# Kernel tuning notes

Measured on AMD Instinct MI355X. Metric: run time of the kernel, lower is better.

Reference implementation:

```python
import jax, jax.numpy as jnp
import numpy as np

N_NODES = 100000


def _gcn_norm(edge_index, num_nodes):
    # PyG GCNConv default: add self-loops, symmetric normalization.
    src, dst = edge_index[0], edge_index[1]
    loop = jnp.arange(num_nodes, dtype=src.dtype)
    src = jnp.concatenate([src, loop])
    dst = jnp.concatenate([dst, loop])
    deg = jax.ops.segment_sum(jnp.ones_like(dst, dtype=jnp.float32), dst,
                              num_segments=num_nodes)
    dinv = jnp.where(deg > 0, jax.lax.rsqrt(jnp.maximum(deg, 1.0)), 0.0)
    norm = dinv[src] * dinv[dst]  # [E + N]
    return src, dst, norm


def _gcn_layer(x, src, dst, norm, W, b, num_nodes):
    h = x @ W                              # [N, out]
    msg = h[src] * norm[:, None]           # gather + scale, [E+N, out]
    agg = jax.ops.segment_sum(msg, dst, num_segments=num_nodes)  # scatter-add
    return agg + b


def setup_inputs() -> dict:
    key = jax.random.key(0)
    ks = jax.random.split(key, 12)
    in_c, hid = 64, 128
    dims = [in_c, hid, hid // 2, hid // 4, hid // 8, 1]
    x = jax.random.normal(ks[0], (N_NODES, in_c), dtype=jnp.float32)
    edge_index = jax.random.randint(ks[1], (2, 1600000), 0, N_NODES,
                                    dtype=jnp.int64)
    inp = {"x": x, "edge_index": edge_index}
    for i in range(5):
        fan_in = dims[i]
        s = 1.0 / np.sqrt(fan_in)
        inp[f"W{i+1}"] = jax.random.uniform(ks[2 + 2 * i], (dims[i], dims[i + 1]),
                                            minval=-s, maxval=s,
                                            dtype=jnp.float32)
        inp[f"b{i+1}"] = jnp.zeros((dims[i + 1],), dtype=jnp.float32)
    return inp


def reference(x, edge_index, W1, b1, W2, b2, W3, b3, W4, b4, W5, b5):
    num_nodes = x.shape[0]
    src, dst, norm = _gcn_norm(edge_index, num_nodes)
    h = _gcn_layer(x, src, dst, norm, W1, b1, num_nodes)
    h = jax.nn.relu(h)
    h = _gcn_layer(h, src, dst, norm, W2, b2, num_nodes)
    h = jax.nn.relu(h)
    h = _gcn_layer(h, src, dst, norm, W3, b3, num_nodes)
    h = jax.nn.relu(h)
    h = _gcn_layer(h, src, dst, norm, W4, b4, num_nodes)
    h = jax.nn.relu(h)
    h = _gcn_layer(h, src, dst, norm, W5, b5, num_nodes)
    return h
```

## Files before the change

### kernel.cpp

```cpp
#include <hip/hip_runtime.h>
#include <math.h>


#define NBIN_MAX 256
#define BSHIFT 9
#define BINW 512
#define CHUNK 2048

__global__ __launch_bounds__(256) void k_hist(const int* __restrict__ dst, int E,
                                              int nbin, int* __restrict__ binCnt) {
    __shared__ int h[NBIN_MAX];
    int t = threadIdx.x;
    for (int i = t; i < nbin; i += 256) h[i] = 0;
    __syncthreads();
    int e4 = (blockIdx.x * 256 + t) * 4;
    int stride = gridDim.x * 256 * 4;
    for (; e4 + 3 < E; e4 += stride) {
        int4 d = *(const int4*)&dst[e4];
        atomicAdd(&h[d.x >> BSHIFT], 1);
        atomicAdd(&h[d.y >> BSHIFT], 1);
        atomicAdd(&h[d.z >> BSHIFT], 1);
        atomicAdd(&h[d.w >> BSHIFT], 1);
    }
    for (; e4 < E; ++e4) atomicAdd(&h[dst[e4] >> BSHIFT], 1);
    __syncthreads();
    for (int i = t; i < nbin; i += 256)
        if (h[i]) atomicAdd(&binCnt[i], h[i]);
}

__global__ __launch_bounds__(256) void k_binscan(const int* __restrict__ binCnt,
                                                 int nbin, int* __restrict__ binBase,
                                                 int* __restrict__ binCur) {
    __shared__ int sh[256];
    int t = threadIdx.x;
    int v = (t < nbin) ? binCnt[t] : 0;
    sh[t] = v;
    __syncthreads();
    for (int d = 1; d < 256; d <<= 1) {
        int u = (t >= d) ? sh[t - d] : 0;
        __syncthreads();
        sh[t] += u;
        __syncthreads();
    }
    int ex = sh[t] - v;
    if (t < nbin) { binBase[t] = ex; binCur[t] = ex; }
    if (t == nbin - 1) binBase[nbin] = sh[t];
}

__global__ __launch_bounds__(256) void k_binfill(const int* __restrict__ src,
                                                 const int* __restrict__ dst, int E,
                                                 int nbin, int* __restrict__ binCur,
                                                 unsigned* __restrict__ tmp) {
    __shared__ int h[NBIN_MAX];
    __shared__ int res[NBIN_MAX];
    int t = threadIdx.x;
    int e0 = blockIdx.x * CHUNK;
    int e1 = min(e0 + CHUNK, E);
    int vend = e0 + ((e1 - e0) & ~3);
    for (int i = t; i < nbin; i += 256) h[i] = 0;
    __syncthreads();
    for (int e = e0 + t * 4; e < vend; e += 1024) {
        int4 d = *(const int4*)&dst[e];
        atomicAdd(&h[d.x >> BSHIFT], 1);
        atomicAdd(&h[d.y >> BSHIFT], 1);
        atomicAdd(&h[d.z >> BSHIFT], 1);
        atomicAdd(&h[d.w >> BSHIFT], 1);
    }
    for (int e = vend + t; e < e1; e += 256)
        atomicAdd(&h[dst[e] >> BSHIFT], 1);
    __syncthreads();
    for (int i = t; i < nbin; i += 256)
        res[i] = h[i] ? atomicAdd(&binCur[i], h[i]) : 0;
    __syncthreads();
    for (int i = t; i < nbin; i += 256) h[i] = 0;
    __syncthreads();
    for (int e = e0 + t * 4; e < vend; e += 1024) {
        int4 d = *(const int4*)&dst[e];
        int4 s = *(const int4*)&src[e];
        int b0 = d.x >> BSHIFT;
        int p0 = res[b0] + atomicAdd(&h[b0], 1);
        tmp[p0] = ((unsigned)s.x << BSHIFT) | (unsigned)(d.x & (BINW - 1));
        int b1 = d.y >> BSHIFT;
        int p1 = res[b1] + atomicAdd(&h[b1], 1);
        tmp[p1] = ((unsigned)s.y << BSHIFT) | (unsigned)(d.y & (BINW - 1));
        int b2 = d.z >> BSHIFT;
        int p2 = res[b2] + atomicAdd(&h[b2], 1);
        tmp[p2] = ((unsigned)s.z << BSHIFT) | (unsigned)(d.z & (BINW - 1));
        int b3 = d.w >> BSHIFT;
        int p3 = res[b3] + atomicAdd(&h[b3], 1);
        tmp[p3] = ((unsigned)s.w << BSHIFT) | (unsigned)(d.w & (BINW - 1));
    }
    for (int e = vend + t; e < e1; e += 256) {
        int d = dst[e];
        int b = d >> BSHIFT;
        int p = res[b] + atomicAdd(&h[b], 1);
        tmp[p] = ((unsigned)src[e] << BSHIFT) | (unsigned)(d & (BINW - 1));
    }
}

__global__ __launch_bounds__(256) void k_csr(const unsigned* __restrict__ tmp,
                                             const int* __restrict__ binBase,
                                             int n, int nbin,
                                             float* __restrict__ dinv,
                                             int* __restrict__ offs,
                                             int* __restrict__ csr) {
    __shared__ int ldeg[BINW];
    __shared__ int loff[BINW];
    __shared__ int pair[256];
    int b = blockIdx.x;
    int t = threadIdx.x;
    ldeg[t] = 0; ldeg[t + 256] = 0;
    __syncthreads();
    int lo = binBase[b], hi = binBase[b + 1];
    for (int p = lo + t; p < hi; p += 256)
        atomicAdd(&ldeg[tmp[p] & (BINW - 1u)], 1);
    __syncthreads();
    int a0 = ldeg[2 * t], a1 = ldeg[2 * t + 1];
    pair[t] = a0 + a1;
    __syncthreads();
    int v = pair[t];
    for (int d = 1; d < 256; d <<= 1) {
        int u = (t >= d) ? pair[t - d] : 0;
        __syncthreads();
        pair[t] += u;
        __syncthreads();
    }
    int ex = pair[t] - v;
    loff[2 * t] = ex;
    loff[2 * t + 1] = ex + a0;
    __syncthreads();
    int v0 = b << BSHIFT;
    for (int i = t; i < BINW; i += 256) {
        int vv = v0 + i;
        if (vv < n) {
            offs[vv] = lo + loff[i];
            dinv[vv] = 1.0f / sqrtf((float)(ldeg[i] + 1));
        }
    }
    if (t == 0 && b == nbin - 1) offs[n] = hi;
    __syncthreads();
    ldeg[t] = 0; ldeg[t + 256] = 0;
    __syncthreads();
    for (int p = lo + t; p < hi; p += 256) {
        unsigned u = tmp[p];
        int d0 = (int)(u & (BINW - 1u));
        int pos = loff[d0] + atomicAdd(&ldeg[d0], 1);
        csr[lo + pos] = (int)(u >> BSHIFT);
    }
}

__global__ __launch_bounds__(256) void k_scale(const float* __restrict__ x,
                                               const float* __restrict__ dinv,
                                               float* __restrict__ xs, int n) {
    int i = blockIdx.x * 256 + threadIdx.x;
    int v = i >> 4;
    if (v >= n) return;
    float4 a = *(const float4*)&x[(size_t)i * 4];
    float dv = dinv[v];
    a.x *= dv; a.y *= dv; a.z *= dv; a.w *= dv;
    *(float4*)&xs[(size_t)i * 4] = a;
}

template <int W, int DEPTH, bool RELU, bool BIAS>
__global__ __launch_bounds__(256) void k_aggv(const float* __restrict__ S,
                                              const float* __restrict__ dinv,
                                              const int* __restrict__ offs,
                                              const int* __restrict__ csr,
                                              const float* __restrict__ bg,
                                              float* __restrict__ Y, int n) {
    constexpr int LPR = W / 4;
    constexpr int G = 64 / LPR;
    int lane = threadIdx.x & 63;
    int wave = threadIdx.x >> 6;
    int v = blockIdx.x * 4 + wave;
    if (v >= n) return;
    int g = lane / LPR;
    int j = lane % LPR;
    float dv = dinv[v];
    float ax0 = 0.f, ay0 = 0.f, az0 = 0.f, aw0 = 0.f;
    float ax1 = 0.f, ay1 = 0.f, az1 = 0.f, aw1 = 0.f;
    if (g == 0) {
        float4 sv = *(const float4*)&S[(size_t)v * W + j * 4];
        ax0 = sv.x; ay0 = sv.y; az0 = sv.z; aw0 = sv.w;
    }
    int e0 = offs[v], re = offs[v + 1];
    int eb = e0;
    for (; eb + G * DEPTH <= re; eb += G * DEPTH) {
        int idx[DEPTH];
#pragma unroll
        for (int d = 0; d < DEPTH; ++d)
            idx[d] = __builtin_nontemporal_load(&csr[eb + d * G + g]);
        float4 buf[DEPTH];
#pragma unroll
        for (int d = 0; d < DEPTH; ++d)
            buf[d] = *(const float4*)&S[(size_t)idx[d] * W + j * 4];
#pragma unroll
        for (int d = 0; d < DEPTH; ++d) {
            if (d & 1) { ax1 += buf[d].x; ay1 += buf[d].y; az1 += buf[d].z; aw1 += buf[d].w; }
            else       { ax0 += buf[d].x; ay0 += buf[d].y; az0 += buf[d].z; aw0 += buf[d].w; }
        }
    }
    for (; eb < re; eb += G) {
        int e = eb + g;
        if (e < re) {
            int u = __builtin_nontemporal_load(&csr[e]);
            float4 a = *(const float4*)&S[(size_t)u * W + j * 4];
            ax0 += a.x; ay0 += a.y; az0 += a.z; aw0 += a.w;
        }
    }
    ax0 += ax1; ay0 += ay1; az0 += az1; aw0 += aw1;
#pragma unroll
    for (int d = LPR; d < 64; d <<= 1) {
        ax0 += __shfl_xor(ax0, d);
        ay0 += __shfl_xor(ay0, d);
        az0 += __shfl_xor(az0, d);
        aw0 += __shfl_xor(aw0, d);
    }
    if (lane < LPR) {
        float4 r;
        r.x = dv * ax0; r.y = dv * ay0; r.z = dv * az0; r.w = dv * aw0;
        if (BIAS) {
            float4 bv = *(const float4*)&bg[j * 4];
            r.x += bv.x; r.y += bv.y; r.z += bv.z; r.w += bv.w;
        }
        if (RELU) {
            r.x = fmaxf(r.x, 0.f); r.y = fmaxf(r.y, 0.f);
            r.z = fmaxf(r.z, 0.f); r.w = fmaxf(r.w, 0.f);
        }
        *(float4*)&Y[(size_t)v * W + j * 4] = r;
    }
}

__global__ __launch_bounds__(256) void k_agg16_gemm5(const float* __restrict__ S,
                                                     const float* __restrict__ dinv,
                                                     const int* __restrict__ offs,
                                                     const int* __restrict__ csr,
                                                     const float* __restrict__ b4,
                                                     const float* __restrict__ W5,
                                                     float* __restrict__ Y, int n) {
    constexpr int W = 16, LPR = 4, G = 16;
    int lane = threadIdx.x & 63;
    int wave = threadIdx.x >> 6;
    int v = blockIdx.x * 4 + wave;
    if (v >= n) return;
    int g = lane / LPR;
    int j = lane % LPR;
    float dv = dinv[v];
    float4 acc0 = make_float4(0.f, 0.f, 0.f, 0.f);
    float4 acc1 = make_float4(0.f, 0.f, 0.f, 0.f);
    if (g == 0) acc0 = *(const float4*)&S[(size_t)v * W + j * 4];
    int e0 = offs[v], re = offs[v + 1];
    for (int eb = e0; eb < re; eb += 2 * G) {
        int ea = eb + g, ec = eb + G + g;
        if (ea < re) {
            int u = csr[ea];
            float4 a = *(const float4*)&S[(size_t)u * W + j * 4];
            acc0.x += a.x; acc0.y += a.y; acc0.z += a.z; acc0.w += a.w;
        }
        if (ec < re) {
            int u = csr[ec];
            float4 a = *(const float4*)&S[(size_t)u * W + j * 4];
            acc1.x += a.x; acc1.y += a.y; acc1.z += a.z; acc1.w += a.w;
        }
    }
    acc0.x += acc1.x; acc0.y += acc1.y; acc0.z += acc1.z; acc0.w += acc1.w;
#pragma unroll
    for (int d = LPR; d < 64; d <<= 1) {
        acc0.x += __shfl_xor(acc0.x, d);
        acc0.y += __shfl_xor(acc0.y, d);
        acc0.z += __shfl_xor(acc0.z, d);
        acc0.w += __shfl_xor(acc0.w, d);
    }
    float4 bv = *(const float4*)&b4[j * 4];
    float4 w5 = *(const float4*)&W5[j * 4];
    float hx = fmaxf(dv * acc0.x + bv.x, 0.f);
    float hy = fmaxf(dv * acc0.y + bv.y, 0.f);
    float hz = fmaxf(dv * acc0.z + bv.z, 0.f);
    float hw = fmaxf(dv * acc0.w + bv.w, 0.f);
    float p = hx * w5.x + hy * w5.y + hz * w5.z + hw * w5.w;
    p += __shfl_xor(p, 1);
    p += __shfl_xor(p, 2);
    if (lane == 0) Y[v] = p * dv;
}

__global__ __launch_bounds__(256) void k_agg1(const float* __restrict__ S,
                                              const float* __restrict__ dinv,
                                              const int* __restrict__ offs,
                                              const int* __restrict__ csr,
                                              const float* __restrict__ bg,
                                              float* __restrict__ Y, int n) {
    int v = blockIdx.x * 256 + threadIdx.x;
    if (v >= n) return;
    float s0 = S[v], s1 = 0.f, s2 = 0.f, s3 = 0.f;
    int e = offs[v], re = offs[v + 1];
    for (; e + 4 <= re; e += 4) {
        int i0 = csr[e], i1 = csr[e + 1], i2 = csr[e + 2], i3 = csr[e + 3];
        s0 += S[i0]; s1 += S[i1]; s2 += S[i2]; s3 += S[i3];
    }
    for (; e < re; ++e) s0 += S[csr[e]];
    Y[v] = dinv[v] * ((s0 + s1) + (s2 + s3)) + bg[0];
}

template <int IN, int OUT, int EPI, int NR>
__global__ __launch_bounds__(256) void k_gemm(const float* __restrict__ X,
                                              const float* __restrict__ Wg,
                                              const float* __restrict__ bg,
                                              const float* __restrict__ dinv,
                                              float* __restrict__ Y, int nrows) {
    constexpr int TPR = OUT / 4;
    constexpr int GROUPS = 256 / TPR;
    constexpr int ROWS = GROUPS * NR;
    __shared__ __align__(16) float Wl[IN * OUT];
    __shared__ __align__(16) float xl[ROWS * IN];
    __shared__ float bl[OUT];
    int tid = threadIdx.x;
    for (int i = tid; i < IN * OUT; i += 256) Wl[i] = Wg[i];
    if (EPI == 0)
        for (int i = tid; i < OUT; i += 256) bl[i] = bg[i];
    int base = blockIdx.x * ROWS;
    for (int i = tid; i < ROWS * IN; i += 256) {
        int r = base + i / IN;
        xl[i] = (r < nrows) ? X[(size_t)base * IN + i] : 0.0f;
    }
    __syncthreads();
    int g = tid / TPR;
    int c0 = (tid % TPR) * 4;
    float4 acc[NR];
#pragma unroll
    for (int r = 0; r < NR; ++r) acc[r] = make_float4(0.f, 0.f, 0.f, 0.f);
#pragma unroll 8
    for (int k = 0; k < IN; ++k) {
        float4 w = *(const float4*)&Wl[k * OUT + c0];
#pragma unroll
        for (int r = 0; r < NR; ++r) {
            float a = xl[(g * NR + r) * IN + k];
            acc[r].x += a * w.x; acc[r].y += a * w.y;
            acc[r].z += a * w.z; acc[r].w += a * w.w;
        }
    }
#pragma unroll
    for (int r = 0; r < NR; ++r) {
        int row = base + g * NR + r;
        if (row >= nrows) continue;
        float4 o = acc[r];
        if (EPI == 0) {
            o.x = fmaxf(o.x + bl[c0], 0.f);
            o.y = fmaxf(o.y + bl[c0 + 1], 0.f);
            o.z = fmaxf(o.z + bl[c0 + 2], 0.f);
            o.w = fmaxf(o.w + bl[c0 + 3], 0.f);
        } else {
            float d0 = dinv[row];
            o.x *= d0; o.y *= d0; o.z *= d0; o.w *= d0;
        }
        *(float4*)&Y[(size_t)row * OUT + c0] = o;
    }
}

extern "C" void kernel_launch(void* const* d_in, const int* in_sizes, int n_in,
                              void* d_out, int out_size, void* d_ws, size_t ws_size,
                              hipStream_t stream) {
    const float* x  = (const float*)d_in[0];
    const int*   ei = (const int*)d_in[1];
    const float* W1 = (const float*)d_in[2];  const float* b1 = (const float*)d_in[3];
    const float* W2 = (const float*)d_in[4];  const float* b2 = (const float*)d_in[5];
    const float* W3 = (const float*)d_in[6];  const float* b3 = (const float*)d_in[7];
    const float* W4 = (const float*)d_in[8];  const float* b4 = (const float*)d_in[9];
    const float* W5 = (const float*)d_in[10]; const float* b5 = (const float*)d_in[11];

    const int N = in_sizes[0] / 64;
    const int E = in_sizes[1] / 2;
    const int* src = ei;
    const int* dst = ei + E;
    const int nbin = (N + BINW - 1) / BINW;

    char* ws = (char*)d_ws;
    size_t off = 0;
    auto alloc = [&](size_t bytes) -> void* {
        void* p = ws + off;
        off = (off + bytes + 255) & ~(size_t)255;
        return p;
    };
    float* dinv    = (float*)alloc((size_t)N * 4);
    int*   offs    = (int*)alloc((size_t)(N + 1) * 4);
    int*   binCnt  = (int*)alloc((size_t)NBIN_MAX * 4);
    int*   binBase = (int*)alloc((size_t)(NBIN_MAX + 1) * 4);
    int*   binCur  = (int*)alloc((size_t)NBIN_MAX * 4);
    int*   csr     = (int*)alloc((size_t)E * 4);
    float* s5      = (float*)alloc((size_t)N * 4);
    float* A       = (float*)alloc((size_t)N * 128 * 4);
    float* B       = (float*)alloc((size_t)N * 64 * 4);
    float* C       = (float*)alloc((size_t)N * 64 * 4);
    unsigned* tmp  = (unsigned*)C;
    float* xs      = A;

    hipMemsetAsync(binCnt, 0, (size_t)NBIN_MAX * 4, stream);

    k_hist<<<256, 256, 0, stream>>>(dst, E, nbin, binCnt);
    k_binscan<<<1, 256, 0, stream>>>(binCnt, nbin, binBase, binCur);
    k_binfill<<<(E + CHUNK - 1) / CHUNK, 256, 0, stream>>>(src, dst, E, nbin, binCur, tmp);
    k_csr<<<nbin, 256, 0, stream>>>(tmp, binBase, N, nbin, dinv, offs, csr);

    const int gagg = (N + 3) / 4;
    k_scale<<<(N * 16 + 255) / 256, 256, 0, stream>>>(x, dinv, xs, N);
    k_aggv<64, 4, false, false><<<gagg, 256, 0, stream>>>(xs, dinv, offs, csr, nullptr, B, N);
    k_gemm<64, 128, 0, 4><<<(N + 31) / 32, 256, 0, stream>>>(B, W1, b1, nullptr, A, N);
    k_gemm<128, 64, 1, 2><<<(N + 31) / 32, 256, 0, stream>>>(A, W2, nullptr, dinv, B, N);
    k_aggv<64, 4, true, true><<<gagg, 256, 0, stream>>>(B, dinv, offs, csr, b2, C, N);
    k_gemm<64, 32, 1, 2><<<(N + 63) / 64, 256, 0, stream>>>(C, W3, nullptr, dinv, B, N);
    k_aggv<32, 2, true, true><<<gagg, 256, 0, stream>>>(B, dinv, offs, csr, b3, A, N);
    k_gemm<32, 16, 1, 2><<<(N + 127) / 128, 256, 0, stream>>>(A, W4, nullptr, dinv, B, N);
    k_agg16_gemm5<<<gagg, 256, 0, stream>>>(B, dinv, offs, csr, b4, W5, s5, N);
    k_agg1<<<(N + 255) / 256, 256, 0, stream>>>(s5, dinv, offs, csr, b5, (float*)d_out, N);
}
```

Baseline: 415.3 us.

## Fuse input scaling into first aggregation and software-pipeline index loads

Removes the separate k_scale pass: the first aggregation now reads raw x and multiplies each gathered row by dinv of its source node, which saves a full N×64 write and read. The aggv inner loop is restructured so the next block's CSR indices are prefetched while the current gathers are in flight, with sched_barrier to hold the ordering. The agg16 kernel is split into an unguarded main loop with nontemporal index loads and a tail loop. The cost is an extra scattered dinv load per edge in layer one and higher register pressure from the prefetched indices.

```diff
diff --git a/kernel.cpp b/kernel.cpp
--- a/kernel.cpp
+++ b/kernel.cpp
@@ -149,19 +149,7 @@
     }
 }
 
-__global__ __launch_bounds__(256) void k_scale(const float* __restrict__ x,
-                                               const float* __restrict__ dinv,
-                                               float* __restrict__ xs, int n) {
-    int i = blockIdx.x * 256 + threadIdx.x;
-    int v = i >> 4;
-    if (v >= n) return;
-    float4 a = *(const float4*)&x[(size_t)i * 4];
-    float dv = dinv[v];
-    a.x *= dv; a.y *= dv; a.z *= dv; a.w *= dv;
-    *(float4*)&xs[(size_t)i * 4] = a;
-}
-
-template <int W, int DEPTH, bool RELU, bool BIAS>
+template <int W, int DEPTH, bool RELU, bool BIAS, bool L1S>
 __global__ __launch_bounds__(256) void k_aggv(const float* __restrict__ S,
                                               const float* __restrict__ dinv,
                                               const int* __restrict__ offs,
@@ -181,23 +169,41 @@
     float ax1 = 0.f, ay1 = 0.f, az1 = 0.f, aw1 = 0.f;
     if (g == 0) {
         float4 sv = *(const float4*)&S[(size_t)v * W + j * 4];
-        ax0 = sv.x; ay0 = sv.y; az0 = sv.z; aw0 = sv.w;
+        float sc = L1S ? dv : 1.0f;
+        ax0 = sv.x * sc; ay0 = sv.y * sc; az0 = sv.z * sc; aw0 = sv.w * sc;
     }
     int e0 = offs[v], re = offs[v + 1];
     int eb = e0;
-    for (; eb + G * DEPTH <= re; eb += G * DEPTH) {
+    int nfull = (re - e0) / (G * DEPTH);
+    if (nfull > 0) {
         int idx[DEPTH];
 #pragma unroll
         for (int d = 0; d < DEPTH; ++d)
             idx[d] = __builtin_nontemporal_load(&csr[eb + d * G + g]);
-        float4 buf[DEPTH];
-#pragma unroll
-        for (int d = 0; d < DEPTH; ++d)
-            buf[d] = *(const float4*)&S[(size_t)idx[d] * W + j * 4];
-#pragma unroll
-        for (int d = 0; d < DEPTH; ++d) {
-            if (d & 1) { ax1 += buf[d].x; ay1 += buf[d].y; az1 += buf[d].z; aw1 += buf[d].w; }
-            else       { ax0 += buf[d].x; ay0 += buf[d].y; az0 += buf[d].z; aw0 += buf[d].w; }
+        for (int b = 1; b <= nfull; ++b) {
+            float4 buf[DEPTH];
+            float dsc[DEPTH];
+#pragma unroll
+            for (int d = 0; d < DEPTH; ++d) {
+                buf[d] = *(const float4*)&S[(size_t)idx[d] * W + j * 4];
+                if (L1S) dsc[d] = dinv[idx[d]];
+            }
+            __builtin_amdgcn_sched_barrier(0);
+            int eb2 = eb + G * DEPTH;
+            if (b < nfull) {
+#pragma unroll
+                for (int d = 0; d < DEPTH; ++d)
+                    idx[d] = __builtin_nontemporal_load(&csr[eb2 + d * G + g]);
+            }
+#pragma unroll
+            for (int d = 0; d < DEPTH; ++d) {
+                float sc = L1S ? dsc[d] : 1.0f;
+                if (d & 1) { ax1 += buf[d].x * sc; ay1 += buf[d].y * sc;
+                             az1 += buf[d].z * sc; aw1 += buf[d].w * sc; }
+                else       { ax0 += buf[d].x * sc; ay0 += buf[d].y * sc;
+                             az0 += buf[d].z * sc; aw0 += buf[d].w * sc; }
+            }
+            eb = eb2;
         }
     }
     for (; eb < re; eb += G) {
@@ -205,7 +211,8 @@
         if (e < re) {
             int u = __builtin_nontemporal_load(&csr[e]);
             float4 a = *(const float4*)&S[(size_t)u * W + j * 4];
-            ax0 += a.x; ay0 += a.y; az0 += a.z; aw0 += a.w;
+            float sc = L1S ? dinv[u] : 1.0f;
+            ax0 += a.x * sc; ay0 += a.y * sc; az0 += a.z * sc; aw0 += a.w * sc;
         }
     }
     ax0 += ax1; ay0 += ay1; az0 += az1; aw0 += aw1;
@@ -250,17 +257,22 @@
     float4 acc1 = make_float4(0.f, 0.f, 0.f, 0.f);
     if (g == 0) acc0 = *(const float4*)&S[(size_t)v * W + j * 4];
     int e0 = offs[v], re = offs[v + 1];
-    for (int eb = e0; eb < re; eb += 2 * G) {
-        int ea = eb + g, ec = eb + G + g;
-        if (ea < re) {
-            int u = csr[ea];
+    int eb = e0;
+    for (; eb + 2 * G <= re; eb += 2 * G) {
+        int u0 = __builtin_nontemporal_load(&csr[eb + g]);
+        int u1 = __builtin_nontemporal_load(&csr[eb + G + g]);
+        float4 a0 = *(const float4*)&S[(size_t)u0 * W + j * 4];
+        float4 a1 = *(const float4*)&S[(size_t)u1 * W + j * 4];
+        __builtin_amdgcn_sched_barrier(0);
+        acc0.x += a0.x; acc0.y += a0.y; acc0.z += a0.z; acc0.w += a0.w;
+        acc1.x += a1.x; acc1.y += a1.y; acc1.z += a1.z; acc1.w += a1.w;
+    }
+    for (; eb < re; eb += G) {
+        int e = eb + g;
+        if (e < re) {
+            int u = __builtin_nontemporal_load(&csr[e]);
             float4 a = *(const float4*)&S[(size_t)u * W + j * 4];
             acc0.x += a.x; acc0.y += a.y; acc0.z += a.z; acc0.w += a.w;
-        }
-        if (ec < re) {
-            int u = csr[ec];
-            float4 a = *(const float4*)&S[(size_t)u * W + j * 4];
-            acc1.x += a.x; acc1.y += a.y; acc1.z += a.z; acc1.w += a.w;
         }
     }
     acc0.x += acc1.x; acc0.y += acc1.y; acc0.z += acc1.z; acc0.w += acc1.w;
@@ -391,7 +403,6 @@
     float* B       = (float*)alloc((size_t)N * 64 * 4);
     float* C       = (float*)alloc((size_t)N * 64 * 4);
     unsigned* tmp  = (unsigned*)C;
-    float* xs      = A;
 
     hipMemsetAsync(binCnt, 0, (size_t)NBIN_MAX * 4, stream);
 
@@ -401,13 +412,12 @@
     k_csr<<<nbin, 256, 0, stream>>>(tmp, binBase, N, nbin, dinv, offs, csr);
 
     const int gagg = (N + 3) / 4;
-    k_scale<<<(N * 16 + 255) / 256, 256, 0, stream>>>(x, dinv, xs, N);
-    k_aggv<64, 4, false, false><<<gagg, 256, 0, stream>>>(xs, dinv, offs, csr, nullptr, B, N);
+    k_aggv<64, 4, false, false, true><<<gagg, 256, 0, stream>>>(x, dinv, offs, csr, nullptr, B, N);
     k_gemm<64, 128, 0, 4><<<(N + 31) / 32, 256, 0, stream>>>(B, W1, b1, nullptr, A, N);
     k_gemm<128, 64, 1, 2><<<(N + 31) / 32, 256, 0, stream>>>(A, W2, nullptr, dinv, B, N);
-    k_aggv<64, 4, true, true><<<gagg, 256, 0, stream>>>(B, dinv, offs, csr, b2, C, N);
+    k_aggv<64, 4, true, true, false><<<gagg, 256, 0, stream>>>(B, dinv, offs, csr, b2, C, N);
     k_gemm<64, 32, 1, 2><<<(N + 63) / 64, 256, 0, stream>>>(C, W3, nullptr, dinv, B, N);
-    k_aggv<32, 2, true, true><<<gagg, 256, 0, stream>>>(B, dinv, offs, csr, b3, A, N);
+    k_aggv<32, 2, true, true, false><<<gagg, 256, 0, stream>>>(B, dinv, offs, csr, b3, A, N);
     k_gemm<32, 16, 1, 2><<<(N + 127) / 128, 256, 0, stream>>>(A, W4, nullptr, dinv, B, N);
     k_agg16_gemm5<<<gagg, 256, 0, stream>>>(B, dinv, offs, csr, b4, W5, s5, N);
     k_agg1<<<(N + 255) / 256, 256, 0, stream>>>(s5, dinv, offs, csr, b5, (float*)d_out, N);
```

After: 412.8 us. Within noise of the previous version (-0.6%).

## Map one lane-group per node in aggregation kernels with software-pipelined gathers

Applied to the files above, without the earlier changes.

Aggregation kernels now assign a group of W/4 lanes to each node instead of a whole wavefront per node. Each group walks the node's whole edge list with double-buffered index loads and row gathers, and the cross-lane shuffle reduction is gone. The first layer's separate dinv pre-scaling kernel is dropped and folded into the aggregation, which now gathers dinv[u] per edge. This cuts wasted lanes on low-degree nodes (about 17 edges each) and one full pass over x. The cost is a serial per-lane edge loop that is exposed to degree imbalance, plus higher register use for the pipeline buffers.

```diff
diff --git a/kernel.cpp b/kernel.cpp
--- a/kernel.cpp
+++ b/kernel.cpp
@@ -149,128 +149,158 @@
     }
 }
 
-__global__ __launch_bounds__(256) void k_scale(const float* __restrict__ x,
-                                               const float* __restrict__ dinv,
-                                               float* __restrict__ xs, int n) {
-    int i = blockIdx.x * 256 + threadIdx.x;
-    int v = i >> 4;
-    if (v >= n) return;
-    float4 a = *(const float4*)&x[(size_t)i * 4];
-    float dv = dinv[v];
-    a.x *= dv; a.y *= dv; a.z *= dv; a.w *= dv;
-    *(float4*)&xs[(size_t)i * 4] = a;
-}
-
-template <int W, int DEPTH, bool RELU, bool BIAS>
-__global__ __launch_bounds__(256) void k_aggv(const float* __restrict__ S,
+template <int W, int DEPTH, bool RELU, bool BIAS, bool L1S>
+__global__ __launch_bounds__(256) void k_aggp(const float* __restrict__ S,
                                               const float* __restrict__ dinv,
                                               const int* __restrict__ offs,
                                               const int* __restrict__ csr,
                                               const float* __restrict__ bg,
                                               float* __restrict__ Y, int n) {
     constexpr int LPR = W / 4;
-    constexpr int G = 64 / LPR;
+    constexpr int GPW = 64 / LPR;
     int lane = threadIdx.x & 63;
     int wave = threadIdx.x >> 6;
-    int v = blockIdx.x * 4 + wave;
+    int grp = lane / LPR;
+    int j = lane % LPR;
+    int v = blockIdx.x * (4 * GPW) + wave * GPW + grp;
     if (v >= n) return;
-    int g = lane / LPR;
-    int j = lane % LPR;
     float dv = dinv[v];
-    float ax0 = 0.f, ay0 = 0.f, az0 = 0.f, aw0 = 0.f;
-    float ax1 = 0.f, ay1 = 0.f, az1 = 0.f, aw1 = 0.f;
-    if (g == 0) {
+    float4 acc0, acc1 = make_float4(0.f, 0.f, 0.f, 0.f);
+    {
         float4 sv = *(const float4*)&S[(size_t)v * W + j * 4];
-        ax0 = sv.x; ay0 = sv.y; az0 = sv.z; aw0 = sv.w;
+        float sc = L1S ? dv : 1.0f;
+        acc0 = make_float4(sv.x * sc, sv.y * sc, sv.z * sc, sv.w * sc);
     }
     int e0 = offs[v], re = offs[v + 1];
-    int eb = e0;
-    for (; eb + G * DEPTH <= re; eb += G * DEPTH) {
-        int idx[DEPTH];
+    int nb = (re - e0) / DEPTH;
+    float4 bA[DEPTH], bB[DEPTH];
+    float dA[DEPTH], dB[DEPTH];
+    int iA[DEPTH], iB[DEPTH];
+    auto loadIdx = [&](int* ix, int base) {
 #pragma unroll
         for (int d = 0; d < DEPTH; ++d)
-            idx[d] = __builtin_nontemporal_load(&csr[eb + d * G + g]);
-        float4 buf[DEPTH];
-#pragma unroll
-        for (int d = 0; d < DEPTH; ++d)
-            buf[d] = *(const float4*)&S[(size_t)idx[d] * W + j * 4];
+            ix[d] = __builtin_nontemporal_load(&csr[base + d]);
+    };
+    auto gather = [&](float4* bf, float* ds, const int* ix) {
 #pragma unroll
         for (int d = 0; d < DEPTH; ++d) {
-            if (d & 1) { ax1 += buf[d].x; ay1 += buf[d].y; az1 += buf[d].z; aw1 += buf[d].w; }
-            else       { ax0 += buf[d].x; ay0 += buf[d].y; az0 += buf[d].z; aw0 += buf[d].w; }
-        }
-    }
-    for (; eb < re; eb += G) {
-        int e = eb + g;
-        if (e < re) {
-            int u = __builtin_nontemporal_load(&csr[e]);
-            float4 a = *(const float4*)&S[(size_t)u * W + j * 4];
-            ax0 += a.x; ay0 += a.y; az0 += a.z; aw0 += a.w;
-        }
-    }
-    ax0 += ax1; ay0 += ay1; az0 += az1; aw0 += aw1;
-#pragma unroll
-    for (int d = LPR; d < 64; d <<= 1) {
-        ax0 += __shfl_xor(ax0, d);
-        ay0 += __shfl_xor(ay0, d);
-        az0 += __shfl_xor(az0, d);
-        aw0 += __shfl_xor(aw0, d);
-    }
-    if (lane < LPR) {
-        float4 r;
-        r.x = dv * ax0; r.y = dv * ay0; r.z = dv * az0; r.w = dv * aw0;
-        if (BIAS) {
-            float4 bv = *(const float4*)&bg[j * 4];
-            r.x += bv.x; r.y += bv.y; r.z += bv.z; r.w += bv.w;
-        }
-        if (RELU) {
-            r.x = fmaxf(r.x, 0.f); r.y = fmaxf(r.y, 0.f);
-            r.z = fmaxf(r.z, 0.f); r.w = fmaxf(r.w, 0.f);
-        }
-        *(float4*)&Y[(size_t)v * W + j * 4] = r;
-    }
-}
-
-__global__ __launch_bounds__(256) void k_agg16_gemm5(const float* __restrict__ S,
-                                                     const float* __restrict__ dinv,
-                                                     const int* __restrict__ offs,
-                                                     const int* __restrict__ csr,
-                                                     const float* __restrict__ b4,
-                                                     const float* __restrict__ W5,
-                                                     float* __restrict__ Y, int n) {
-    constexpr int W = 16, LPR = 4, G = 16;
+            bf[d] = *(const float4*)&S[(size_t)ix[d] * W + j * 4];
+            if (L1S) ds[d] = dinv[ix[d]];
+        }
+    };
+    auto consume = [&](const float4* bf, const float* ds) {
+#pragma unroll
+        for (int d = 0; d < DEPTH; ++d) {
+            float sc = L1S ? ds[d] : 1.0f;
+            if (d & 1) { acc1.x += bf[d].x * sc; acc1.y += bf[d].y * sc;
+                         acc1.z += bf[d].z * sc; acc1.w += bf[d].w * sc; }
+            else       { acc0.x += bf[d].x * sc; acc0.y += bf[d].y * sc;
+                         acc0.z += bf[d].z * sc; acc0.w += bf[d].w * sc; }
+        }
+    };
+    if (nb >= 1) {
+        loadIdx(iA, e0);
+        gather(bA, dA, iA);
+        if (nb >= 2) loadIdx(iB, e0 + DEPTH);
+        int b = 0;
+        while (b + 2 <= nb) {
+            gather(bB, dB, iB);
+            if (b + 2 < nb) loadIdx(iA, e0 + (b + 2) * DEPTH);
+            consume(bA, dA);
+            if (b + 2 < nb) {
+                gather(bA, dA, iA);
+                if (b + 3 < nb) loadIdx(iB, e0 + (b + 3) * DEPTH);
+            }
+            consume(bB, dB);
+            b += 2;
+        }
+        if (b < nb) consume(bA, dA);
+    }
+    for (int k = e0 + nb * DEPTH; k < re; ++k) {
+        int u = __builtin_nontemporal_load(&csr[k]);
+        float4 a = *(const float4*)&S[(size_t)u * W + j * 4];
+        float sc = L1S ? dinv[u] : 1.0f;
+        acc0.x += a.x * sc; acc0.y += a.y * sc; acc0.z += a.z * sc; acc0.w += a.w * sc;
+    }
+    acc0.x += acc1.x; acc0.y += acc1.y; acc0.z += acc1.z; acc0.w += acc1.w;
+    float4 r;
+    r.x = dv * acc0.x; r.y = dv * acc0.y; r.z = dv * acc0.z; r.w = dv * acc0.w;
+    if (BIAS) {
+        float4 bv = *(const float4*)&bg[j * 4];
+        r.x += bv.x; r.y += bv.y; r.z += bv.z; r.w += bv.w;
+    }
+    if (RELU) {
+        r.x = fmaxf(r.x, 0.f); r.y = fmaxf(r.y, 0.f);
+        r.z = fmaxf(r.z, 0.f); r.w = fmaxf(r.w, 0.f);
+    }
+    *(float4*)&Y[(size_t)v * W + j * 4] = r;
+}
+
+template <int DEPTH>
+__global__ __launch_bounds__(256) void k_agg16g5(const float* __restrict__ S,
+                                                 const float* __restrict__ dinv,
+                                                 const int* __restrict__ offs,
+                                                 const int* __restrict__ csr,
+                                                 const float* __restrict__ b4,
+                                                 const float* __restrict__ W5,
+                                                 float* __restrict__ Y, int n) {
+    constexpr int W = 16, LPR = 4, GPW = 16;
     int lane = threadIdx.x & 63;
     int wave = threadIdx.x >> 6;
-    int v = blockIdx.x * 4 + wave;
+    int grp = lane / LPR;
+    int j = lane % LPR;
+    int v = blockIdx.x * (4 * GPW) + wave * GPW + grp;
     if (v >= n) return;
-    int g = lane / LPR;
-    int j = lane % LPR;
     float dv = dinv[v];
-    float4 acc0 = make_float4(0.f, 0.f, 0.f, 0.f);
+    float4 acc0 = *(const float4*)&S[(size_t)v * W + j * 4];
     float4 acc1 = make_float4(0.f, 0.f, 0.f, 0.f);
-    if (g == 0) acc0 = *(const float4*)&S[(size_t)v * W + j * 4];
     int e0 = offs[v], re = offs[v + 1];
-    for (int eb = e0; eb < re; eb += 2 * G) {
-        int ea = eb + g, ec = eb + G + g;
-        if (ea < re) {
-            int u = csr[ea];
-            float4 a = *(const float4*)&S[(size_t)u * W + j * 4];
-            acc0.x += a.x; acc0.y += a.y; acc0.z += a.z; acc0.w += a.w;
-        }
-        if (ec < re) {
-            int u = csr[ec];
-            float4 a = *(const float4*)&S[(size_t)u * W + j * 4];
-            acc1.x += a.x; acc1.y += a.y; acc1.z += a.z; acc1.w += a.w;
-        }
+    int nb = (re - e0) / DEPTH;
+    float4 bA[DEPTH], bB[DEPTH];
+    int iA[DEPTH], iB[DEPTH];
+    auto loadIdx = [&](int* ix, int base) {
+#pragma unroll
+        for (int d = 0; d < DEPTH; ++d)
+            ix[d] = __builtin_nontemporal_load(&csr[base + d]);
+    };
+    auto gather = [&](float4* bf, const int* ix) {
+#pragma unroll
+        for (int d = 0; d < DEPTH; ++d)
+            bf[d] = *(const float4*)&S[(size_t)ix[d] * W + j * 4];
+    };
+    auto consume = [&](const float4* bf) {
+#pragma unroll
+        for (int d = 0; d < DEPTH; ++d) {
+            if (d & 1) { acc1.x += bf[d].x; acc1.y += bf[d].y;
+                         acc1.z += bf[d].z; acc1.w += bf[d].w; }
+            else       { acc0.x += bf[d].x; acc0.y += bf[d].y;
+                         acc0.z += bf[d].z; acc0.w += bf[d].w; }
+        }
+    };
+    if (nb >= 1) {
+        loadIdx(iA, e0);
+        gather(bA, iA);
+        if (nb >= 2) loadIdx(iB, e0 + DEPTH);
+        int b = 0;
+        while (b + 2 <= nb) {
+            gather(bB, iB);
+            if (b + 2 < nb) loadIdx(iA, e0 + (b + 2) * DEPTH);
+            consume(bA);
+            if (b + 2 < nb) {
+                gather(bA, iA);
+                if (b + 3 < nb) loadIdx(iB, e0 + (b + 3) * DEPTH);
+            }
+            consume(bB);
+            b += 2;
+        }
+        if (b < nb) consume(bA);
+    }
+    for (int k = e0 + nb * DEPTH; k < re; ++k) {
+        int u = __builtin_nontemporal_load(&csr[k]);
+        float4 a = *(const float4*)&S[(size_t)u * W + j * 4];
+        acc0.x += a.x; acc0.y += a.y; acc0.z += a.z; acc0.w += a.w;
     }
     acc0.x += acc1.x; acc0.y += acc1.y; acc0.z += acc1.z; acc0.w += acc1.w;
-#pragma unroll
-    for (int d = LPR; d < 64; d <<= 1) {
-        acc0.x += __shfl_xor(acc0.x, d);
-        acc0.y += __shfl_xor(acc0.y, d);
-        acc0.z += __shfl_xor(acc0.z, d);
-        acc0.w += __shfl_xor(acc0.w, d);
-    }
     float4 bv = *(const float4*)&b4[j * 4];
     float4 w5 = *(const float4*)&W5[j * 4];
     float hx = fmaxf(dv * acc0.x + bv.x, 0.f);
@@ -280,7 +310,7 @@
     float p = hx * w5.x + hy * w5.y + hz * w5.z + hw * w5.w;
     p += __shfl_xor(p, 1);
     p += __shfl_xor(p, 2);
-    if (lane == 0) Y[v] = p * dv;
+    if (j == 0) Y[v] = p * dv;
 }
 
 __global__ __launch_bounds__(256) void k_agg1(const float* __restrict__ S,
@@ -391,7 +421,6 @@
     float* B       = (float*)alloc((size_t)N * 64 * 4);
     float* C       = (float*)alloc((size_t)N * 64 * 4);
     unsigned* tmp  = (unsigned*)C;
-    float* xs      = A;
 
     hipMemsetAsync(binCnt, 0, (size_t)NBIN_MAX * 4, stream);
 
@@ -400,15 +429,13 @@
     k_binfill<<<(E + CHUNK - 1) / CHUNK, 256, 0, stream>>>(src, dst, E, nbin, binCur, tmp);
     k_csr<<<nbin, 256, 0, stream>>>(tmp, binBase, N, nbin, dinv, offs, csr);
 
-    const int gagg = (N + 3) / 4;
-    k_scale<<<(N * 16 + 255) / 256, 256, 0, stream>>>(x, dinv, xs, N);
-    k_aggv<64, 4, false, false><<<gagg, 256, 0, stream>>>(xs, dinv, offs, csr, nullptr, B, N);
+    k_aggp<64, 3, false, false, true><<<(N + 15) / 16, 256, 0, stream>>>(x, dinv, offs, csr, nullptr, B, N);
     k_gemm<64, 128, 0, 4><<<(N + 31) / 32, 256, 0, stream>>>(B, W1, b1, nullptr, A, N);
     k_gemm<128, 64, 1, 2><<<(N + 31) / 32, 256, 0, stream>>>(A, W2, nullptr, dinv, B, N);
-    k_aggv<64, 4, true, true><<<gagg, 256, 0, stream>>>(B, dinv, offs, csr, b2, C, N);
+    k_aggp<64, 4, true, true, false><<<(N + 15) / 16, 256, 0, stream>>>(B, dinv, offs, csr, b2, C, N);
     k_gemm<64, 32, 1, 2><<<(N + 63) / 64, 256, 0, stream>>>(C, W3, nullptr, dinv, B, N);
-    k_aggv<32, 2, true, true><<<gagg, 256, 0, stream>>>(B, dinv, offs, csr, b3, A, N);
+    k_aggp<32, 4, true, true, false><<<(N + 31) / 32, 256, 0, stream>>>(B, dinv, offs, csr, b3, A, N);
     k_gemm<32, 16, 1, 2><<<(N + 127) / 128, 256, 0, stream>>>(A, W4, nullptr, dinv, B, N);
-    k_agg16_gemm5<<<gagg, 256, 0, stream>>>(B, dinv, offs, csr, b4, W5, s5, N);
+    k_agg16g5<4><<<(N + 63) / 64, 256, 0, stream>>>(B, dinv, offs, csr, b4, W5, s5, N);
     k_agg1<<<(N + 255) / 256, 256, 0, stream>>>(s5, dinv, offs, csr, b5, (float*)d_out, N);
 }
```

Result: faster. 391.1 us (-5.8%).

## Aggregate per destination bin with LDS atomics and edge-balanced partitioning

Applied to the files above, without the earlier changes.

Replaces the one-wave-per-node CSR gather kernels with bin-based kernels. Each block owns 128 destination nodes, splits that bin's edges evenly across thread groups, run-length merges consecutive edges with the same destination, and accumulates into an LDS tile with shared-memory atomics. The CSR entries now pack source and local destination together, the first layer folds in source scaling instead of running a separate scale kernel, and the GEMM's x tile gets padding to avoid bank conflicts. The goal is load balance and avoiding idle lanes on low-degree nodes, at the cost of LDS atomic contention, fewer blocks (about 782), and larger LDS use per block.

```diff
diff --git a/kernel.cpp b/kernel.cpp
--- a/kernel.cpp
+++ b/kernel.cpp
@@ -2,9 +2,9 @@
 #include <math.h>
 
 
-#define NBIN_MAX 256
-#define BSHIFT 9
-#define BINW 512
+#define NBIN_MAX 1024
+#define BSHIFT 7
+#define BINW 128
 #define CHUNK 2048
 
 __global__ __launch_bounds__(256) void k_hist(const int* __restrict__ dst, int E,
@@ -33,8 +33,15 @@
                                                  int* __restrict__ binCur) {
     __shared__ int sh[256];
     int t = threadIdx.x;
-    int v = (t < nbin) ? binCnt[t] : 0;
-    sh[t] = v;
+    int loc[4];
+    int s = 0;
+#pragma unroll
+    for (int i = 0; i < 4; ++i) {
+        int idx = t * 4 + i;
+        int v = (idx < nbin) ? binCnt[idx] : 0;
+        loc[i] = s; s += v;
+    }
+    sh[t] = s;
     __syncthreads();
     for (int d = 1; d < 256; d <<= 1) {
         int u = (t >= d) ? sh[t - d] : 0;
@@ -42,9 +49,13 @@
         sh[t] += u;
         __syncthreads();
     }
-    int ex = sh[t] - v;
-    if (t < nbin) { binBase[t] = ex; binCur[t] = ex; }
-    if (t == nbin - 1) binBase[nbin] = sh[t];
+    int ex = sh[t] - s;
+#pragma unroll
+    for (int i = 0; i < 4; ++i) {
+        int idx = t * 4 + i;
+        if (idx < nbin) { binBase[idx] = ex + loc[i]; binCur[idx] = ex + loc[i]; }
+    }
+    if (t == 255) binBase[nbin] = sh[255];
 }
 
 __global__ __launch_bounds__(256) void k_binfill(const int* __restrict__ src,
@@ -105,182 +116,206 @@
                                              int* __restrict__ offs,
                                              int* __restrict__ csr) {
     __shared__ int ldeg[BINW];
+    __shared__ int sc[BINW];
     __shared__ int loff[BINW];
-    __shared__ int pair[256];
     int b = blockIdx.x;
     int t = threadIdx.x;
-    ldeg[t] = 0; ldeg[t + 256] = 0;
+    if (t < BINW) ldeg[t] = 0;
     __syncthreads();
     int lo = binBase[b], hi = binBase[b + 1];
     for (int p = lo + t; p < hi; p += 256)
         atomicAdd(&ldeg[tmp[p] & (BINW - 1u)], 1);
     __syncthreads();
-    int a0 = ldeg[2 * t], a1 = ldeg[2 * t + 1];
-    pair[t] = a0 + a1;
-    __syncthreads();
-    int v = pair[t];
-    for (int d = 1; d < 256; d <<= 1) {
-        int u = (t >= d) ? pair[t - d] : 0;
+    if (t < BINW) sc[t] = ldeg[t];
+    __syncthreads();
+    for (int d = 1; d < BINW; d <<= 1) {
+        int u = 0;
+        if (t < BINW && t >= d) u = sc[t - d];
         __syncthreads();
-        pair[t] += u;
+        if (t < BINW) sc[t] += u;
         __syncthreads();
     }
-    int ex = pair[t] - v;
-    loff[2 * t] = ex;
-    loff[2 * t + 1] = ex + a0;
+    if (t < BINW) loff[t] = sc[t] - ldeg[t];
     __syncthreads();
     int v0 = b << BSHIFT;
-    for (int i = t; i < BINW; i += 256) {
-        int vv = v0 + i;
+    if (t < BINW) {
+        int vv = v0 + t;
         if (vv < n) {
-            offs[vv] = lo + loff[i];
-            dinv[vv] = 1.0f / sqrtf((float)(ldeg[i] + 1));
+            offs[vv] = lo + loff[t];
+            dinv[vv] = 1.0f / sqrtf((float)(ldeg[t] + 1));
         }
     }
     if (t == 0 && b == nbin - 1) offs[n] = hi;
     __syncthreads();
-    ldeg[t] = 0; ldeg[t + 256] = 0;
+    if (t < BINW) ldeg[t] = 0;
     __syncthreads();
     for (int p = lo + t; p < hi; p += 256) {
         unsigned u = tmp[p];
         int d0 = (int)(u & (BINW - 1u));
         int pos = loff[d0] + atomicAdd(&ldeg[d0], 1);
-        csr[lo + pos] = (int)(u >> BSHIFT);
-    }
-}
-
-__global__ __launch_bounds__(256) void k_scale(const float* __restrict__ x,
-                                               const float* __restrict__ dinv,
-                                               float* __restrict__ xs, int n) {
-    int i = blockIdx.x * 256 + threadIdx.x;
-    int v = i >> 4;
-    if (v >= n) return;
-    float4 a = *(const float4*)&x[(size_t)i * 4];
-    float dv = dinv[v];
-    a.x *= dv; a.y *= dv; a.z *= dv; a.w *= dv;
-    *(float4*)&xs[(size_t)i * 4] = a;
-}
-
-template <int W, int DEPTH, bool RELU, bool BIAS>
-__global__ __launch_bounds__(256) void k_aggv(const float* __restrict__ S,
+        csr[lo + pos] = (int)u;
+    }
+}
+
+template <int W, bool L1S, bool RELU, bool BIAS>
+__global__ __launch_bounds__(256) void k_aggb(const float* __restrict__ S,
                                               const float* __restrict__ dinv,
-                                              const int* __restrict__ offs,
+                                              const int* __restrict__ binBase,
                                               const int* __restrict__ csr,
                                               const float* __restrict__ bg,
                                               float* __restrict__ Y, int n) {
-    constexpr int LPR = W / 4;
-    constexpr int G = 64 / LPR;
-    int lane = threadIdx.x & 63;
-    int wave = threadIdx.x >> 6;
-    int v = blockIdx.x * 4 + wave;
-    if (v >= n) return;
-    int g = lane / LPR;
-    int j = lane % LPR;
-    float dv = dinv[v];
-    float ax0 = 0.f, ay0 = 0.f, az0 = 0.f, aw0 = 0.f;
-    float ax1 = 0.f, ay1 = 0.f, az1 = 0.f, aw1 = 0.f;
-    if (g == 0) {
-        float4 sv = *(const float4*)&S[(size_t)v * W + j * 4];
-        ax0 = sv.x; ay0 = sv.y; az0 = sv.z; aw0 = sv.w;
-    }
-    int e0 = offs[v], re = offs[v + 1];
-    int eb = e0;
-    for (; eb + G * DEPTH <= re; eb += G * DEPTH) {
-        int idx[DEPTH];
-#pragma unroll
-        for (int d = 0; d < DEPTH; ++d)
-            idx[d] = __builtin_nontemporal_load(&csr[eb + d * G + g]);
-        float4 buf[DEPTH];
-#pragma unroll
-        for (int d = 0; d < DEPTH; ++d)
-            buf[d] = *(const float4*)&S[(size_t)idx[d] * W + j * 4];
-#pragma unroll
-        for (int d = 0; d < DEPTH; ++d) {
-            if (d & 1) { ax1 += buf[d].x; ay1 += buf[d].y; az1 += buf[d].z; aw1 += buf[d].w; }
-            else       { ax0 += buf[d].x; ay0 += buf[d].y; az0 += buf[d].z; aw0 += buf[d].w; }
-        }
-    }
-    for (; eb < re; eb += G) {
-        int e = eb + g;
-        if (e < re) {
-            int u = __builtin_nontemporal_load(&csr[e]);
-            float4 a = *(const float4*)&S[(size_t)u * W + j * 4];
-            ax0 += a.x; ay0 += a.y; az0 += a.z; aw0 += a.w;
-        }
-    }
-    ax0 += ax1; ay0 += ay1; az0 += az1; aw0 += aw1;
-#pragma unroll
-    for (int d = LPR; d < 64; d <<= 1) {
-        ax0 += __shfl_xor(ax0, d);
-        ay0 += __shfl_xor(ay0, d);
-        az0 += __shfl_xor(az0, d);
-        aw0 += __shfl_xor(aw0, d);
-    }
-    if (lane < LPR) {
+    constexpr int LPE = W / 4;
+    constexpr int GR = 256 / LPE;
+    constexpr int ACCS = W + 4;
+    __shared__ __align__(16) float accL[BINW * ACCS];
+    int t = threadIdx.x;
+    int b = blockIdx.x;
+    for (int i = t; i < BINW * ACCS / 4; i += 256)
+        ((float4*)accL)[i] = make_float4(0.f, 0.f, 0.f, 0.f);
+    __syncthreads();
+    int lo = binBase[b], hi = binBase[b + 1];
+    int g = t / LPE, j = t % LPE;
+    int total = hi - lo;
+    int gs = lo + (int)((long long)total * g / GR);
+    int ge = lo + (int)((long long)total * (g + 1) / GR);
+    int rd = -1;
+    float4 rv = make_float4(0.f, 0.f, 0.f, 0.f);
+    auto flush = [&]() {
+        if (rd >= 0) {
+            atomicAdd(&accL[rd * ACCS + 4 * j + 0], rv.x);
+            atomicAdd(&accL[rd * ACCS + 4 * j + 1], rv.y);
+            atomicAdd(&accL[rd * ACCS + 4 * j + 2], rv.z);
+            atomicAdd(&accL[rd * ACCS + 4 * j + 3], rv.w);
+        }
+    };
+    int e = gs;
+    for (; e + 8 <= ge; e += 8) {
+        unsigned pk[8];
+#pragma unroll
+        for (int d = 0; d < 8; ++d) pk[d] = (unsigned)csr[e + d];
+        float4 gv[8];
+        float scb[8];
+#pragma unroll
+        for (int d = 0; d < 8; ++d) {
+            int s = (int)(pk[d] >> BSHIFT);
+            gv[d] = *(const float4*)&S[(size_t)s * W + j * 4];
+            if (L1S) scb[d] = dinv[s];
+        }
+#pragma unroll
+        for (int d = 0; d < 8; ++d) {
+            float4 val = gv[d];
+            if (L1S) { val.x *= scb[d]; val.y *= scb[d]; val.z *= scb[d]; val.w *= scb[d]; }
+            int dl = (int)(pk[d] & (BINW - 1u));
+            if (dl != rd) { flush(); rd = dl; rv = val; }
+            else { rv.x += val.x; rv.y += val.y; rv.z += val.z; rv.w += val.w; }
+        }
+    }
+    for (; e < ge; ++e) {
+        unsigned u = (unsigned)csr[e];
+        int s = (int)(u >> BSHIFT);
+        float4 val = *(const float4*)&S[(size_t)s * W + j * 4];
+        if (L1S) { float q = dinv[s]; val.x *= q; val.y *= q; val.z *= q; val.w *= q; }
+        int dl = (int)(u & (BINW - 1u));
+        if (dl != rd) { flush(); rd = dl; rv = val; }
+        else { rv.x += val.x; rv.y += val.y; rv.z += val.z; rv.w += val.w; }
+    }
+    flush();
+    __syncthreads();
+    int v0 = b << BSHIFT;
+    for (int i = t; i < BINW * LPE; i += 256) {
+        int row = i / LPE, jj = i % LPE;
+        int v = v0 + row;
+        if (v >= n) continue;
+        float dv = dinv[v];
+        float4 a = *(float4*)&accL[row * ACCS + jj * 4];
+        float4 sv = *(const float4*)&S[(size_t)v * W + jj * 4];
+        float ssc = L1S ? dv : 1.0f;
         float4 r;
-        r.x = dv * ax0; r.y = dv * ay0; r.z = dv * az0; r.w = dv * aw0;
+        r.x = dv * (a.x + sv.x * ssc);
+        r.y = dv * (a.y + sv.y * ssc);
+        r.z = dv * (a.z + sv.z * ssc);
+        r.w = dv * (a.w + sv.w * ssc);
         if (BIAS) {
-            float4 bv = *(const float4*)&bg[j * 4];
+            float4 bv = *(const float4*)&bg[jj * 4];
             r.x += bv.x; r.y += bv.y; r.z += bv.z; r.w += bv.w;
         }
         if (RELU) {
             r.x = fmaxf(r.x, 0.f); r.y = fmaxf(r.y, 0.f);
             r.z = fmaxf(r.z, 0.f); r.w = fmaxf(r.w, 0.f);
         }
-        *(float4*)&Y[(size_t)v * W + j * 4] = r;
-    }
-}
-
-__global__ __launch_bounds__(256) void k_agg16_gemm5(const float* __restrict__ S,
-                                                     const float* __restrict__ dinv,
-                                                     const int* __restrict__ offs,
-                                                     const int* __restrict__ csr,
-                                                     const float* __restrict__ b4,
-                                                     const float* __restrict__ W5,
-                                                     float* __restrict__ Y, int n) {
-    constexpr int W = 16, LPR = 4, G = 16;
-    int lane = threadIdx.x & 63;
-    int wave = threadIdx.x >> 6;
-    int v = blockIdx.x * 4 + wave;
-    if (v >= n) return;
-    int g = lane / LPR;
-    int j = lane % LPR;
-    float dv = dinv[v];
-    float4 acc0 = make_float4(0.f, 0.f, 0.f, 0.f);
-    float4 acc1 = make_float4(0.f, 0.f, 0.f, 0.f);
-    if (g == 0) acc0 = *(const float4*)&S[(size_t)v * W + j * 4];
-    int e0 = offs[v], re = offs[v + 1];
-    for (int eb = e0; eb < re; eb += 2 * G) {
-        int ea = eb + g, ec = eb + G + g;
-        if (ea < re) {
-            int u = csr[ea];
-            float4 a = *(const float4*)&S[(size_t)u * W + j * 4];
-            acc0.x += a.x; acc0.y += a.y; acc0.z += a.z; acc0.w += a.w;
-        }
-        if (ec < re) {
-            int u = csr[ec];
-            float4 a = *(const float4*)&S[(size_t)u * W + j * 4];
-            acc1.x += a.x; acc1.y += a.y; acc1.z += a.z; acc1.w += a.w;
-        }
-    }
-    acc0.x += acc1.x; acc0.y += acc1.y; acc0.z += acc1.z; acc0.w += acc1.w;
-#pragma unroll
-    for (int d = LPR; d < 64; d <<= 1) {
-        acc0.x += __shfl_xor(acc0.x, d);
-        acc0.y += __shfl_xor(acc0.y, d);
-        acc0.z += __shfl_xor(acc0.z, d);
-        acc0.w += __shfl_xor(acc0.w, d);
-    }
-    float4 bv = *(const float4*)&b4[j * 4];
-    float4 w5 = *(const float4*)&W5[j * 4];
-    float hx = fmaxf(dv * acc0.x + bv.x, 0.f);
-    float hy = fmaxf(dv * acc0.y + bv.y, 0.f);
-    float hz = fmaxf(dv * acc0.z + bv.z, 0.f);
-    float hw = fmaxf(dv * acc0.w + bv.w, 0.f);
-    float p = hx * w5.x + hy * w5.y + hz * w5.z + hw * w5.w;
-    p += __shfl_xor(p, 1);
-    p += __shfl_xor(p, 2);
-    if (lane == 0) Y[v] = p * dv;
+        *(float4*)&Y[(size_t)v * W + jj * 4] = r;
+    }
+}
+
+__global__ __launch_bounds__(256) void k_aggb16g5(const float* __restrict__ S,
+                                                  const float* __restrict__ dinv,
+                                                  const int* __restrict__ binBase,
+                                                  const int* __restrict__ csr,
+                                                  const float* __restrict__ b4,
+                                                  const float* __restrict__ W5,
+                                                  float* __restrict__ Y, int n) {
+    constexpr int W = 16, LPE = 4, GR = 64, ACCS = 20;
+    __shared__ __align__(16) float accL[BINW * ACCS];
+    int t = threadIdx.x;
+    int b = blockIdx.x;
+    for (int i = t; i < BINW * ACCS / 4; i += 256)
+        ((float4*)accL)[i] = make_float4(0.f, 0.f, 0.f, 0.f);
+    __syncthreads();
+    int lo = binBase[b], hi = binBase[b + 1];
+    int g = t / LPE, j = t % LPE;
+    int total = hi - lo;
+    int gs = lo + (int)((long long)total * g / GR);
+    int ge = lo + (int)((long long)total * (g + 1) / GR);
+    int rd = -1;
+    float4 rv = make_float4(0.f, 0.f, 0.f, 0.f);
+    auto flush = [&]() {
+        if (rd >= 0) {
+            atomicAdd(&accL[rd * ACCS + 4 * j + 0], rv.x);
+            atomicAdd(&accL[rd * ACCS + 4 * j + 1], rv.y);
+            atomicAdd(&accL[rd * ACCS + 4 * j + 2], rv.z);
+            atomicAdd(&accL[rd * ACCS + 4 * j + 3], rv.w);
+        }
+    };
+    int e = gs;
+    for (; e + 8 <= ge; e += 8) {
+        unsigned pk[8];
+#pragma unroll
+        for (int d = 0; d < 8; ++d) pk[d] = (unsigned)csr[e + d];
+        float4 gv[8];
+#pragma unroll
+        for (int d = 0; d < 8; ++d)
+            gv[d] = *(const float4*)&S[(size_t)(pk[d] >> BSHIFT) * W + j * 4];
+#pragma unroll
+        for (int d = 0; d < 8; ++d) {
+            int dl = (int)(pk[d] & (BINW - 1u));
+            if (dl != rd) { flush(); rd = dl; rv = gv[d]; }
+            else { rv.x += gv[d].x; rv.y += gv[d].y; rv.z += gv[d].z; rv.w += gv[d].w; }
+        }
+    }
+    for (; e < ge; ++e) {
+        unsigned u = (unsigned)csr[e];
+        float4 val = *(const float4*)&S[(size_t)(u >> BSHIFT) * W + j * 4];
+        int dl = (int)(u & (BINW - 1u));
+        if (dl != rd) { flush(); rd = dl; rv = val; }
+        else { rv.x += val.x; rv.y += val.y; rv.z += val.z; rv.w += val.w; }
+    }
+    flush();
+    __syncthreads();
+    int v0 = b << BSHIFT;
+    if (t < BINW) {
+        int v = v0 + t;
+        if (v < n) {
+            float dv = dinv[v];
+            float p = 0.f;
+#pragma unroll
+            for (int c = 0; c < 16; ++c) {
+                float h = dv * (accL[t * ACCS + c] + S[(size_t)v * 16 + c]) + b4[c];
+                h = fmaxf(h, 0.f);
+                p += h * W5[c];
+            }
+            Y[v] = p * dv;
+        }
+    }
 }
 
 __global__ __launch_bounds__(256) void k_agg1(const float* __restrict__ S,
@@ -294,10 +329,13 @@
     float s0 = S[v], s1 = 0.f, s2 = 0.f, s3 = 0.f;
     int e = offs[v], re = offs[v + 1];
     for (; e + 4 <= re; e += 4) {
-        int i0 = csr[e], i1 = csr[e + 1], i2 = csr[e + 2], i3 = csr[e + 3];
+        int i0 = (int)((unsigned)csr[e] >> BSHIFT);
+        int i1 = (int)((unsigned)csr[e + 1] >> BSHIFT);
+        int i2 = (int)((unsigned)csr[e + 2] >> BSHIFT);
+        int i3 = (int)((unsigned)csr[e + 3] >> BSHIFT);
         s0 += S[i0]; s1 += S[i1]; s2 += S[i2]; s3 += S[i3];
     }
-    for (; e < re; ++e) s0 += S[csr[e]];
+    for (; e < re; ++e) s0 += S[(unsigned)csr[e] >> BSHIFT];
     Y[v] = dinv[v] * ((s0 + s1) + (s2 + s3)) + bg[0];
 }
 
@@ -310,8 +348,9 @@
     constexpr int TPR = OUT / 4;
     constexpr int GROUPS = 256 / TPR;
     constexpr int ROWS = GROUPS * NR;
+    constexpr int XS = IN + 1;
     __shared__ __align__(16) float Wl[IN * OUT];
-    __shared__ __align__(16) float xl[ROWS * IN];
+    __shared__ float xl[ROWS * XS];
     __shared__ float bl[OUT];
     int tid = threadIdx.x;
     for (int i = tid; i < IN * OUT; i += 256) Wl[i] = Wg[i];
@@ -319,8 +358,9 @@
         for (int i = tid; i < OUT; i += 256) bl[i] = bg[i];
     int base = blockIdx.x * ROWS;
     for (int i = tid; i < ROWS * IN; i += 256) {
-        int r = base + i / IN;
-        xl[i] = (r < nrows) ? X[(size_t)base * IN + i] : 0.0f;
+        int r = i / IN, c = i % IN;
+        int row = base + r;
+        xl[r * XS + c] = (row < nrows) ? X[(size_t)base * IN + i] : 0.0f;
     }
     __syncthreads();
     int g = tid / TPR;
@@ -333,7 +373,7 @@
         float4 w = *(const float4*)&Wl[k * OUT + c0];
 #pragma unroll
         for (int r = 0; r < NR; ++r) {
-            float a = xl[(g * NR + r) * IN + k];
+            float a = xl[(g * NR + r) * XS + k];
             acc[r].x += a * w.x; acc[r].y += a * w.y;
             acc[r].z += a * w.z; acc[r].w += a * w.w;
         }
@@ -391,7 +431,6 @@
     float* B       = (float*)alloc((size_t)N * 64 * 4);
     float* C       = (float*)alloc((size_t)N * 64 * 4);
     unsigned* tmp  = (unsigned*)C;
-    float* xs      = A;
 
     hipMemsetAsync(binCnt, 0, (size_t)NBIN_MAX * 4, stream);
 
@@ -400,15 +439,13 @@
     k_binfill<<<(E + CHUNK - 1) / CHUNK, 256, 0, stream>>>(src, dst, E, nbin, binCur, tmp);
     k_csr<<<nbin, 256, 0, stream>>>(tmp, binBase, N, nbin, dinv, offs, csr);
 
-    const int gagg = (N + 3) / 4;
-    k_scale<<<(N * 16 + 255) / 256, 256, 0, stream>>>(x, dinv, xs, N);
-    k_aggv<64, 4, false, false><<<gagg, 256, 0, stream>>>(xs, dinv, offs, csr, nullptr, B, N);
+    k_aggb<64, true, false, false><<<nbin, 256, 0, stream>>>(x, dinv, binBase, csr, nullptr, B, N);
     k_gemm<64, 128, 0, 4><<<(N + 31) / 32, 256, 0, stream>>>(B, W1, b1, nullptr, A, N);
     k_gemm<128, 64, 1, 2><<<(N + 31) / 32, 256, 0, stream>>>(A, W2, nullptr, dinv, B, N);
-    k_aggv<64, 4, true, true><<<gagg, 256, 0, stream>>>(B, dinv, offs, csr, b2, C, N);
+    k_aggb<64, false, true, true><<<nbin, 256, 0, stream>>>(B, dinv, binBase, csr, b2, C, N);
     k_gemm<64, 32, 1, 2><<<(N + 63) / 64, 256, 0, stream>>>(C, W3, nullptr, dinv, B, N);
-    k_aggv<32, 2, true, true><<<gagg, 256, 0, stream>>>(B, dinv, offs, csr, b3, A, N);
+    k_aggb<32, false, true, true><<<nbin, 256, 0, stream>>>(B, dinv, binBase, csr, b3, A, N);
     k_gemm<32, 16, 1, 2><<<(N + 127) / 128, 256, 0, stream>>>(A, W4, nullptr, dinv, B, N);
-    k_agg16_gemm5<<<gagg, 256, 0, stream>>>(B, dinv, offs, csr, b4, W5, s5, N);
+    k_aggb16g5<<<nbin, 256, 0, stream>>>(B, dinv, binBase, csr, b4, W5, s5, N);
     k_agg1<<<(N + 255) / 256, 256, 0, stream>>>(s5, dinv, offs, csr, b5, (float*)d_out, N);
 }
```

Result: no change. 414.9 us (-0.1%).
